# Kernel tuning notes

Measured on AMD Instinct MI355X. Metric: run time of the kernel, lower is better.

Reference implementation:

```python
import jax, jax.numpy as jnp
import numpy as np

EPS = 1e-5
DN = ('NCHW', 'OIHW', 'NCHW')

def _conv(x, w):
    return jax.lax.conv_general_dilated(x, w, (1, 1), 'VALID', dimension_numbers=DN)

def _bn4(x, g, b, m, v):
    # BatchNorm2d in eval mode, per-channel over NCHW
    inv = g / jnp.sqrt(v + EPS)
    return x * inv[None, :, None, None] + (b - m * inv)[None, :, None, None]

def _bn1(x, g, b, m, v):
    inv = g / jnp.sqrt(v + EPS)
    return x * inv[None, :] + (b - m * inv)[None, :]

def _hardtanh(x):
    return jnp.clip(x, -1.0, 1.0)

def _sign(x):
    return jnp.sign(x)

def _maxpool2(x):
    return jax.lax.reduce_window(x, -jnp.inf, jax.lax.max,
                                 (1, 1, 2, 2), (1, 1, 2, 2), 'VALID')

def setup_inputs() -> dict:
    key = jax.random.key(0)
    ks = jax.random.split(key, 20)
    B = 8192
    d = {
        'x': jax.random.normal(ks[0], (B, 8, 16, 16), jnp.float32),
        'w0': jax.random.normal(ks[1], (32, 8, 3, 3), jnp.float32) * 0.1,
        'b0': jax.random.normal(ks[2], (32,), jnp.float32) * 0.1,
        'g1': jax.random.uniform(ks[3], (32,), jnp.float32, 0.5, 1.5),
        'be1': jax.random.normal(ks[4], (32,), jnp.float32) * 0.1,
        'm1': jax.random.normal(ks[5], (32,), jnp.float32) * 0.1,
        'v1': jax.random.uniform(ks[6], (32,), jnp.float32, 0.5, 1.5),
        'w2': jax.random.normal(ks[7], (32, 32, 3, 3), jnp.float32) * 0.1,
        'g2': jax.random.uniform(ks[8], (32,), jnp.float32, 0.5, 1.5),
        'be2': jax.random.normal(ks[9], (32,), jnp.float32) * 0.1,
        'm2': jax.random.normal(ks[10], (32,), jnp.float32) * 0.1,
        'v2': jax.random.uniform(ks[11], (32,), jnp.float32, 0.5, 1.5),
        'w_fc': jax.random.normal(ks[12], (516, 1152), jnp.float32) * 0.03,
        'g3': jax.random.uniform(ks[13], (516,), jnp.float32, 0.5, 1.5),
        'be3': jax.random.normal(ks[14], (516,), jnp.float32) * 0.1,
        'm3': jax.random.normal(ks[15], (516,), jnp.float32) * 0.1,
        'v3': jax.random.uniform(ks[16], (516,), jnp.float32, 0.5, 1.5),
        'w_last': jax.random.normal(ks[17], (10, 516), jnp.float32) * 0.05,
        'b_last': jax.random.normal(ks[18], (10,), jnp.float32) * 0.05,
    }
    return d

def reference(x, w0, b0, g1, be1, m1, v1, w2, g2, be2, m2, v2,
              w_fc, g3, be3, m3, v3, w_last, b_last):
    # initial float conv + BN + Hardtanh
    h = _conv(x, w0) + b0[None, :, None, None]          # [B,32,14,14]
    h = _hardtanh(_bn4(h, g1, be1, m1, v1))
    # binarized conv (sign(input), sign(weight), no bias)
    h = _conv(_sign(h), _sign(w2))                      # [B,32,12,12]
    h = _hardtanh(_bn4(h, g2, be2, m2, v2))
    h = _maxpool2(h)                                    # [B,32,6,6]
    # dropout is identity in eval mode
    h = h.reshape(h.shape[0], -1)                       # [B,1152]
    # binarized linear (no bias)
    h = _sign(h) @ _sign(w_fc).T                        # [B,516]
    h = _hardtanh(_bn1(h, g3, be3, m3, v3))
    return h @ w_last.T + b_last[None, :]               # [B,10]
```

## Files before the change

kernel.cpp:

```cpp
#include <hip/hip_runtime.h>
#include <cstdint>

#define EPSF 1e-5f

typedef __attribute__((ext_vector_type(8))) short short8;
typedef __attribute__((ext_vector_type(4))) float f32x4;
typedef __attribute__((ext_vector_type(4))) unsigned int u32x4;

__device__ inline uint32_t bf16rne(float x) {
    uint32_t u = __builtin_bit_cast(uint32_t, x);
    return (u + 0x7fffu + ((u >> 16) & 1u)) >> 16;
}
__device__ inline float bf16f(uint32_t b) {
    return __builtin_bit_cast(float, b << 16);
}

__global__ __launch_bounds__(256) void prep_kernel(
    const float* __restrict__ w2, const float* __restrict__ wfc,
    const float* __restrict__ g3, const float* __restrict__ be3,
    const float* __restrict__ m3, const float* __restrict__ v3,
    const float* __restrict__ wlast,
    const float* __restrict__ w0, const float* __restrict__ b0,
    const float* __restrict__ g1, const float* __restrict__ be1,
    const float* __restrict__ m1, const float* __restrict__ v1,
    uint32_t* __restrict__ w2bits, uint32_t* __restrict__ wfcb,
    float* __restrict__ inv3p, float* __restrict__ sh3p, float* __restrict__ wlt,
    uint32_t* __restrict__ bfrag, float2* __restrict__ bn1c)
{
    int id = blockIdx.x * 256 + threadIdx.x;
    if (id < 288) {
        int co = id / 9, r = id % 9;
        uint32_t b = 0;
        for (int ci = 0; ci < 32; ci++)
            b |= (uint32_t)(w2[(co * 32 + ci) * 9 + r] < 0.f) << ci;
        w2bits[id] = b;
        return;
    }
    id -= 288;
    if (id < 36 * 576) {
        int j = id / 36, pos = id % 36;
        uint32_t b = 0;
        if (j < 516) {
            const float* row = wfc + j * 1152 + pos;
            for (int c = 0; c < 32; c++)
                b |= (uint32_t)(row[c * 36] < 0.f) << c;
        }
        wfcb[pos * 576 + j] = b;
        return;
    }
    id -= 36 * 576;
    if (id < 576) {
        float iv = 0.f, sh = 0.f;
        if (id < 516) {
            iv = g3[id] / sqrtf(__fadd_rn(v3[id], EPSF));
            sh = __fsub_rn(be3[id], __fmul_rn(m3[id], iv));
        }
        inv3p[id] = iv; sh3p[id] = sh;
        return;
    }
    id -= 576;
    if (id < 5760) {
        int k = id / 576, j = id % 576;
        wlt[id] = (j < 516) ? wlast[k * 516 + j] : 0.f;
        return;
    }
    id -= 5760;
    if (id < 768) {
        int L = id / 12, r = id % 12;
        int nt = r / 6, s = (r % 6) / 2, h = r & 1;
        int g = L >> 4, n = L & 15;
        int tap = 4 * s + g;
        uint32_t d[4] = {0, 0, 0, 0};
        if (tap < 9) {
            int co = nt * 16 + n;
            for (int j2 = 0; j2 < 4; j2++) {
                float wa = w0[co * 72 + (2 * j2) * 9 + tap];
                float wb = w0[co * 72 + (2 * j2 + 1) * 9 + tap];
                uint32_t ha = bf16rne(wa), hb = bf16rne(wb);
                uint32_t va, vb;
                if (h == 0) { va = ha; vb = hb; }
                else { va = bf16rne(wa - bf16f(ha)); vb = bf16rne(wb - bf16f(hb)); }
                d[j2] = va | (vb << 16);
            }
        }
        *(u32x4*)(bfrag + id * 4) = (u32x4){d[0], d[1], d[2], d[3]};
        return;
    }
    id -= 768;
    if (id < 32) {
        float iv = g1[id] / sqrtf(__fadd_rn(v1[id], EPSF));
        float sh = __fsub_rn(be1[id], __fmul_rn(m1[id], iv));
        float off = __fadd_rn(__fmul_rn(b0[id], iv), sh);
        bn1c[id] = make_float2(iv, off);
    }
}

__device__ __noinline__ bool recheck_sign(const float* __restrict__ xim,
                                          const float* __restrict__ w0,
                                          int py, int px, int co,
                                          float ivc, float offc)
{
    double ad = 0.0;
    for (int ci = 0; ci < 8; ci++)
        for (int ky = 0; ky < 3; ky++)
            for (int kx = 0; kx < 3; kx++)
                ad = fma((double)xim[ci * 256 + (py + ky) * 16 + px + kx],
                         (double)w0[co * 72 + ci * 9 + ky * 3 + kx], ad);
    return (ad * (double)ivc + (double)offc) < 0.0;
}

__global__ __launch_bounds__(128, 4) void convAB(
    const float* __restrict__ x, const float* __restrict__ w0,
    const uint32_t* __restrict__ bfrag, const float2* __restrict__ bn1c,
    const uint32_t* __restrict__ w2bits,
    const float* __restrict__ g2, const float* __restrict__ be2,
    const float* __restrict__ m2, const float* __restrict__ v2,
    uint32_t* __restrict__ fcin)
{
    __shared__ __align__(16) char simg[9216];
    __shared__ __align__(8) uint32_t s1l[196];

    const int t = threadIdx.x;
    const int wv = t >> 6, lane = t & 63;
    const int img = blockIdx.x;
    const float* xim = x + img * 2048;
    char* hib = simg;
    char* lob = simg + 4608;

    const int g = lane >> 4;
    const int n = lane & 15;

    short8 Bh[2][3], Bl[2][3];
    {
        const uint32_t* bb = bfrag + lane * 48;
        #pragma unroll
        for (int nt = 0; nt < 2; nt++)
            #pragma unroll
            for (int s = 0; s < 3; s++) {
                Bh[nt][s] = *(const short8*)(bb + (nt * 6 + s * 2) * 4);
                Bl[nt][s] = *(const short8*)(bb + (nt * 6 + s * 2 + 1) * 4);
            }
    }
    const float2 bnA = bn1c[n], bnB = bn1c[16 + n];

    #pragma unroll
    for (int qq = 0; qq < 2; qq++) {
        int pos = lane + 64 * (2 * wv + qq);
        uint32_t hw[4], lw[4];
        #pragma unroll
        for (int j2 = 0; j2 < 4; j2++) {
            float a = xim[(2 * j2) * 256 + pos];
            float b = xim[(2 * j2 + 1) * 256 + pos];
            uint32_t ha = bf16rne(a), hb = bf16rne(b);
            uint32_t la = bf16rne(a - bf16f(ha)), lb = bf16rne(b - bf16f(hb));
            hw[j2] = ha | (hb << 16);
            lw[j2] = la | (lb << 16);
        }
        *(u32x4*)(hib + pos * 16) = (u32x4){hw[0], hw[1], hw[2], hw[3]};
        *(u32x4*)(lob + pos * 16) = (u32x4){lw[0], lw[1], lw[2], lw[3]};
    }
    if (lane < 32) {
        char* gp = (wv == 0) ? hib : lob;
        *(u32x4*)(gp + (256 + lane) * 16) = (u32x4){0, 0, 0, 0};
    }

    int koff[3];
    #pragma unroll
    for (int s = 0; s < 3; s++) {
        int tap = 4 * s + g;
        koff[s] = (tap < 9) ? ((tap / 3) * 16 + (tap % 3)) * 16 : 0;
    }

    __syncthreads();

    for (int tile = wv; tile < 13; tile += 2) {
        int posA = tile * 16 + n;
        int pyA = posA / 14, pxA = posA - pyA * 14;
        int sl = (pyA * 16 + pxA) * 16;

        f32x4 acc0 = {0.f, 0.f, 0.f, 0.f}, acc1 = {0.f, 0.f, 0.f, 0.f};
        #pragma unroll
        for (int s = 0; s < 3; s++) {
            short8 Ah = *(const short8*)(hib + sl + koff[s]);
            short8 Al = *(const short8*)(lob + sl + koff[s]);
            acc0 = __builtin_amdgcn_mfma_f32_16x16x32_bf16(Al, Bh[0][s], acc0, 0, 0, 0);
            acc0 = __builtin_amdgcn_mfma_f32_16x16x32_bf16(Ah, Bl[0][s], acc0, 0, 0, 0);
            acc0 = __builtin_amdgcn_mfma_f32_16x16x32_bf16(Ah, Bh[0][s], acc0, 0, 0, 0);
            acc1 = __builtin_amdgcn_mfma_f32_16x16x32_bf16(Al, Bh[1][s], acc1, 0, 0, 0);
            acc1 = __builtin_amdgcn_mfma_f32_16x16x32_bf16(Ah, Bl[1][s], acc1, 0, 0, 0);
            acc1 = __builtin_amdgcn_mfma_f32_16x16x32_bf16(Ah, Bh[1][s], acc1, 0, 0, 0);
        }

        #pragma unroll
        for (int r = 0; r < 4; r++) {
            int pos = tile * 16 + 4 * g + r;
            float yv0 = fmaf(acc0[r], bnA.x, bnA.y);
            float yv1 = fmaf(acc1[r], bnB.x, bnB.y);
            bool bit0, bit1;
            if (__builtin_expect(pos < 196 && fabsf(yv0) < 3e-4f, 0)) {
                int py = pos / 14, px = pos - py * 14;
                bit0 = recheck_sign(xim, w0, py, px, n, bnA.x, bnA.y);
            } else bit0 = (yv0 < 0.f);
            if (__builtin_expect(pos < 196 && fabsf(yv1) < 3e-4f, 0)) {
                int py = pos / 14, px = pos - py * 14;
                bit1 = recheck_sign(xim, w0, py, px, 16 + n, bnB.x, bnB.y);
            } else bit1 = (yv1 < 0.f);
            unsigned long long m0 = __ballot(bit0);
            unsigned long long m1 = __ballot(bit1);
            uint32_t word = (uint32_t)((m0 >> (16 * g)) & 0xffffull)
                          | ((uint32_t)((m1 >> (16 * g)) & 0xffffull) << 16);
            if (n == 0 && pos < 196) s1l[pos] = word;
        }
    }

    __syncthreads();

    {
        const int c = lane & 31, h = lane >> 5;
        uint32_t wr[9];
        #pragma unroll
        for (int k = 0; k < 9; k++) wr[k] = w2bits[c * 9 + k];
        float ivv = g2[c] / sqrtf(__fadd_rn(v2[c], EPSF));
        float shv = __fsub_rn(be2[c], __fmul_rn(m2[c], ivv));
        uint32_t* outp = fcin + img * 36;
        const int cb0 = 6 * h;

        for (int yy = 0; yy < 3; yy++) {
            const int y2 = 3 * wv + yy;
            const int rbase = 2 * y2 * 14;
            uint32_t win[4][4];
            #pragma unroll
            for (int rr = 0; rr < 4; rr++) {
                uint2 a = *(const uint2*)&s1l[rbase + rr * 14 + cb0];
                uint2 b = *(const uint2*)&s1l[rbase + rr * 14 + cb0 + 2];
                win[rr][0] = a.x; win[rr][1] = a.y; win[rr][2] = b.x; win[rr][3] = b.y;
            }
            for (int step = 0; step < 3; step++) {
                if (step > 0) {
                    #pragma unroll
                    for (int rr = 0; rr < 4; rr++) {
                        win[rr][0] = win[rr][2]; win[rr][1] = win[rr][3];
                        uint2 b = *(const uint2*)&s1l[rbase + rr * 14 + cb0 + 2 * step + 2];
                        win[rr][2] = b.x; win[rr][3] = b.y;
                    }
                }
                int mx = -10000;
                #pragma unroll
                for (int dy = 0; dy < 2; dy++)
                    #pragma unroll
                    for (int dx = 0; dx < 2; dx++) {
                        int p = 0;
                        #pragma unroll
                        for (int ky = 0; ky < 3; ky++)
                            #pragma unroll
                            for (int kx = 0; kx < 3; kx++)
                                p += __popc(win[dy + ky][dx + kx] ^ wr[ky * 3 + kx]);
                        mx = max(mx, 288 - 2 * p);
                    }
                float yv = __fadd_rn(__fmul_rn((float)mx, ivv), shv);
                unsigned long long mb = __ballot(yv < 0.f);
                if (lane == 0)  outp[y2 * 6 + step]     = (uint32_t)mb;
                if (lane == 32) outp[y2 * 6 + step + 3] = (uint32_t)(mb >> 32);
            }
        }
    }
}

__global__ __launch_bounds__(256) void fcC(
    const uint32_t* __restrict__ fcin, const uint32_t* __restrict__ wfcb,
    const float* __restrict__ inv3p, const float* __restrict__ sh3p,
    const float* __restrict__ wlt, const float* __restrict__ blast,
    float* __restrict__ out)
{
    __shared__ uint32_t l_in[288];
    const int t = threadIdx.x, wid = t >> 6, lane = t & 63;

    for (int i = t; i < 288; i += 256) l_in[i] = fcin[blockIdx.x * 288 + i];
    __syncthreads();

    const int b0i = blockIdx.x * 8 + wid * 2;
    const uint32_t* in0 = &l_in[wid * 72];

    int pc0[9], pc1[9];
    #pragma unroll
    for (int q = 0; q < 9; q++) { pc0[q] = 0; pc1[q] = 0; }

    for (int w = 0; w < 36; w++) {
        uint32_t i0 = in0[w], i1 = in0[36 + w];
        const uint32_t* wf = wfcb + w * 576 + lane;
        #pragma unroll
        for (int q = 0; q < 9; q++) {
            uint32_t f = wf[q * 64];
            pc0[q] += __popc(i0 ^ f);
            pc1[q] += __popc(i1 ^ f);
        }
    }

    float oa[2][10];
    #pragma unroll
    for (int b = 0; b < 2; b++)
        #pragma unroll
        for (int k = 0; k < 10; k++) oa[b][k] = 0.f;

    #pragma unroll
    for (int q = 0; q < 9; q++) {
        int j = lane + 64 * q;
        float ivv = inv3p[j], shv = sh3p[j];
        float t0 = fminf(1.f, fmaxf(-1.f, __fadd_rn(__fmul_rn((float)(1152 - 2 * pc0[q]), ivv), shv)));
        float t1 = fminf(1.f, fmaxf(-1.f, __fadd_rn(__fmul_rn((float)(1152 - 2 * pc1[q]), ivv), shv)));
        #pragma unroll
        for (int k = 0; k < 10; k++) {
            float wv = wlt[k * 576 + j];
            oa[0][k] = fmaf(t0, wv, oa[0][k]);
            oa[1][k] = fmaf(t1, wv, oa[1][k]);
        }
    }

    #pragma unroll
    for (int m = 1; m < 64; m <<= 1)
        #pragma unroll
        for (int b = 0; b < 2; b++)
            #pragma unroll
            for (int k = 0; k < 10; k++)
                oa[b][k] += __shfl_xor(oa[b][k], m, 64);

    if (lane == 0) {
        for (int b = 0; b < 2; b++)
            for (int k = 0; k < 10; k++)
                out[(b0i + b) * 10 + k] = oa[b][k] + blast[k];
    }
}

extern "C" void kernel_launch(void* const* d_in, const int* in_sizes, int n_in,
                              void* d_out, int out_size, void* d_ws, size_t ws_size,
                              hipStream_t stream)
{
    (void)in_sizes; (void)n_in; (void)out_size; (void)ws_size;
    const float* x     = (const float*)d_in[0];
    const float* w0    = (const float*)d_in[1];
    const float* b0    = (const float*)d_in[2];
    const float* g1    = (const float*)d_in[3];
    const float* be1   = (const float*)d_in[4];
    const float* m1    = (const float*)d_in[5];
    const float* v1    = (const float*)d_in[6];
    const float* w2    = (const float*)d_in[7];
    const float* g2    = (const float*)d_in[8];
    const float* be2   = (const float*)d_in[9];
    const float* m2    = (const float*)d_in[10];
    const float* v2    = (const float*)d_in[11];
    const float* wfc   = (const float*)d_in[12];
    const float* g3    = (const float*)d_in[13];
    const float* be3   = (const float*)d_in[14];
    const float* m3    = (const float*)d_in[15];
    const float* v3    = (const float*)d_in[16];
    const float* wlast = (const float*)d_in[17];
    const float* blast = (const float*)d_in[18];

    char* ws = (char*)d_ws;
    uint32_t* fcin   = (uint32_t*)(ws + 6422528);
    uint32_t* w2bits = (uint32_t*)(ws + 7602176);
    uint32_t* wfcb   = (uint32_t*)(ws + 7603328);
    float*    inv3p  = (float*)(ws + 7686272);
    float*    sh3p   = (float*)(ws + 7688576);
    float*    wlt    = (float*)(ws + 7690880);
    uint32_t* bfrag  = (uint32_t*)(ws + 7713920);
    float2*   bn1c   = (float2*)(ws + 7726208);

    prep_kernel<<<110, 256, 0, stream>>>(w2, wfc, g3, be3, m3, v3, wlast,
                                         w0, b0, g1, be1, m1, v1,
                                         w2bits, wfcb, inv3p, sh3p, wlt,
                                         bfrag, bn1c);
    convAB<<<8192, 128, 0, stream>>>(x, w0, bfrag, bn1c,
                                     w2bits, g2, be2, m2, v2, fcin);
    fcC<<<1024, 256, 0, stream>>>(fcin, wfcb, inv3p, sh3p, wlt, blast, (float*)d_out);
}
```

Measured before the change: 215.0 us.

## Process four images per block with double-buffered async global-to-LDS prefetch

The conv kernel now loops over four images per block instead of one. It prefetches the next image's raw input into a second LDS buffer with global_load_lds while the current image runs through the MFMA and popcount stages. This is meant to hide global load latency and spread the per-block B-fragment and BN setup over more work. In exchange it adds LDS use, launches fewer blocks, and relies on correct wait semantics for the asynchronous LDS loads.

```diff
diff --git a/kernel.cpp b/kernel.cpp
--- a/kernel.cpp
+++ b/kernel.cpp
@@ -13,6 +13,13 @@
 }
 __device__ inline float bf16f(uint32_t b) {
     return __builtin_bit_cast(float, b << 16);
+}
+
+__device__ inline void gl_lds16(const void* g, void* l) {
+    __builtin_amdgcn_global_load_lds(
+        (__attribute__((address_space(1))) void*)(uintptr_t)(g),
+        (__attribute__((address_space(3))) void*)(l),
+        16, 0, 0);
 }
 
 __global__ __launch_bounds__(256) void prep_kernel(
@@ -118,12 +125,11 @@
     uint32_t* __restrict__ fcin)
 {
     __shared__ __align__(16) char simg[9216];
+    __shared__ __align__(16) uint32_t rawb[2][2048];
     __shared__ __align__(8) uint32_t s1l[196];
 
     const int t = threadIdx.x;
     const int wv = t >> 6, lane = t & 63;
-    const int img = blockIdx.x;
-    const float* xim = x + img * 2048;
     char* hib = simg;
     char* lob = simg + 4608;
 
@@ -143,22 +149,6 @@
     }
     const float2 bnA = bn1c[n], bnB = bn1c[16 + n];
 
-    #pragma unroll
-    for (int qq = 0; qq < 2; qq++) {
-        int pos = lane + 64 * (2 * wv + qq);
-        uint32_t hw[4], lw[4];
-        #pragma unroll
-        for (int j2 = 0; j2 < 4; j2++) {
-            float a = xim[(2 * j2) * 256 + pos];
-            float b = xim[(2 * j2 + 1) * 256 + pos];
-            uint32_t ha = bf16rne(a), hb = bf16rne(b);
-            uint32_t la = bf16rne(a - bf16f(ha)), lb = bf16rne(b - bf16f(hb));
-            hw[j2] = ha | (hb << 16);
-            lw[j2] = la | (lb << 16);
-        }
-        *(u32x4*)(hib + pos * 16) = (u32x4){hw[0], hw[1], hw[2], hw[3]};
-        *(u32x4*)(lob + pos * 16) = (u32x4){lw[0], lw[1], lw[2], lw[3]};
-    }
     if (lane < 32) {
         char* gp = (wv == 0) ? hib : lob;
         *(u32x4*)(gp + (256 + lane) * 16) = (u32x4){0, 0, 0, 0};
@@ -171,98 +161,144 @@
         koff[s] = (tap < 9) ? ((tap / 3) * 16 + (tap % 3)) * 16 : 0;
     }
 
-    __syncthreads();
-
-    for (int tile = wv; tile < 13; tile += 2) {
-        int posA = tile * 16 + n;
-        int pyA = posA / 14, pxA = posA - pyA * 14;
-        int sl = (pyA * 16 + pxA) * 16;
-
-        f32x4 acc0 = {0.f, 0.f, 0.f, 0.f}, acc1 = {0.f, 0.f, 0.f, 0.f};
-        #pragma unroll
-        for (int s = 0; s < 3; s++) {
-            short8 Ah = *(const short8*)(hib + sl + koff[s]);
-            short8 Al = *(const short8*)(lob + sl + koff[s]);
-            acc0 = __builtin_amdgcn_mfma_f32_16x16x32_bf16(Al, Bh[0][s], acc0, 0, 0, 0);
-            acc0 = __builtin_amdgcn_mfma_f32_16x16x32_bf16(Ah, Bl[0][s], acc0, 0, 0, 0);
-            acc0 = __builtin_amdgcn_mfma_f32_16x16x32_bf16(Ah, Bh[0][s], acc0, 0, 0, 0);
-            acc1 = __builtin_amdgcn_mfma_f32_16x16x32_bf16(Al, Bh[1][s], acc1, 0, 0, 0);
-            acc1 = __builtin_amdgcn_mfma_f32_16x16x32_bf16(Ah, Bl[1][s], acc1, 0, 0, 0);
-            acc1 = __builtin_amdgcn_mfma_f32_16x16x32_bf16(Ah, Bh[1][s], acc1, 0, 0, 0);
-        }
-
-        #pragma unroll
-        for (int r = 0; r < 4; r++) {
-            int pos = tile * 16 + 4 * g + r;
-            float yv0 = fmaf(acc0[r], bnA.x, bnA.y);
-            float yv1 = fmaf(acc1[r], bnB.x, bnB.y);
-            bool bit0, bit1;
-            if (__builtin_expect(pos < 196 && fabsf(yv0) < 3e-4f, 0)) {
-                int py = pos / 14, px = pos - py * 14;
-                bit0 = recheck_sign(xim, w0, py, px, n, bnA.x, bnA.y);
-            } else bit0 = (yv0 < 0.f);
-            if (__builtin_expect(pos < 196 && fabsf(yv1) < 3e-4f, 0)) {
-                int py = pos / 14, px = pos - py * 14;
-                bit1 = recheck_sign(xim, w0, py, px, 16 + n, bnB.x, bnB.y);
-            } else bit1 = (yv1 < 0.f);
-            unsigned long long m0 = __ballot(bit0);
-            unsigned long long m1 = __ballot(bit1);
-            uint32_t word = (uint32_t)((m0 >> (16 * g)) & 0xffffull)
-                          | ((uint32_t)((m1 >> (16 * g)) & 0xffffull) << 16);
-            if (n == 0 && pos < 196) s1l[pos] = word;
-        }
-    }
-
-    __syncthreads();
-
     {
-        const int c = lane & 31, h = lane >> 5;
-        uint32_t wr[9];
-        #pragma unroll
-        for (int k = 0; k < 9; k++) wr[k] = w2bits[c * 9 + k];
-        float ivv = g2[c] / sqrtf(__fadd_rn(v2[c], EPSF));
-        float shv = __fsub_rn(be2[c], __fmul_rn(m2[c], ivv));
-        uint32_t* outp = fcin + img * 36;
-        const int cb0 = 6 * h;
-
-        for (int yy = 0; yy < 3; yy++) {
-            const int y2 = 3 * wv + yy;
-            const int rbase = 2 * y2 * 14;
-            uint32_t win[4][4];
-            #pragma unroll
-            for (int rr = 0; rr < 4; rr++) {
-                uint2 a = *(const uint2*)&s1l[rbase + rr * 14 + cb0];
-                uint2 b = *(const uint2*)&s1l[rbase + rr * 14 + cb0 + 2];
-                win[rr][0] = a.x; win[rr][1] = a.y; win[rr][2] = b.x; win[rr][3] = b.y;
-            }
-            for (int step = 0; step < 3; step++) {
-                if (step > 0) {
+        const float* xg = x + (size_t)(blockIdx.x * 4) * 2048;
+        #pragma unroll
+        for (int j = 0; j < 4; j++)
+            gl_lds16(xg + (wv * 4 + j) * 256 + lane * 4,
+                     (char*)&rawb[0][(wv * 4 + j) * 256]);
+    }
+
+    int cur = 0;
+    for (int i = 0; i < 4; ++i) {
+        const int img = blockIdx.x * 4 + i;
+        const float* xim = x + (size_t)img * 2048;
+
+        __syncthreads();
+
+        {
+            const uint32_t* rp = rawb[cur];
+            #pragma unroll
+            for (int qq = 0; qq < 2; qq++) {
+                int pos = lane + 64 * (2 * wv + qq);
+                uint32_t hw[4], lw[4];
+                #pragma unroll
+                for (int j2 = 0; j2 < 4; j2++) {
+                    float a = __builtin_bit_cast(float, rp[(2 * j2) * 256 + pos]);
+                    float b = __builtin_bit_cast(float, rp[(2 * j2 + 1) * 256 + pos]);
+                    uint32_t ha = bf16rne(a), hb = bf16rne(b);
+                    uint32_t la = bf16rne(a - bf16f(ha)), lb = bf16rne(b - bf16f(hb));
+                    hw[j2] = ha | (hb << 16);
+                    lw[j2] = la | (lb << 16);
+                }
+                *(u32x4*)(hib + pos * 16) = (u32x4){hw[0], hw[1], hw[2], hw[3]};
+                *(u32x4*)(lob + pos * 16) = (u32x4){lw[0], lw[1], lw[2], lw[3]};
+            }
+        }
+
+        __syncthreads();
+
+        if (i < 3) {
+            const float* xg = x + (size_t)(img + 1) * 2048;
+            #pragma unroll
+            for (int j = 0; j < 4; j++)
+                gl_lds16(xg + (wv * 4 + j) * 256 + lane * 4,
+                         (char*)&rawb[cur ^ 1][(wv * 4 + j) * 256]);
+        }
+
+        for (int tile = wv; tile < 13; tile += 2) {
+            int posA = tile * 16 + n;
+            int pyA = posA / 14, pxA = posA - pyA * 14;
+            int sl = (pyA * 16 + pxA) * 16;
+
+            f32x4 acc0 = {0.f, 0.f, 0.f, 0.f}, acc1 = {0.f, 0.f, 0.f, 0.f};
+            #pragma unroll
+            for (int s = 0; s < 3; s++) {
+                short8 Ah = *(const short8*)(hib + sl + koff[s]);
+                short8 Al = *(const short8*)(lob + sl + koff[s]);
+                acc0 = __builtin_amdgcn_mfma_f32_16x16x32_bf16(Al, Bh[0][s], acc0, 0, 0, 0);
+                acc0 = __builtin_amdgcn_mfma_f32_16x16x32_bf16(Ah, Bl[0][s], acc0, 0, 0, 0);
+                acc0 = __builtin_amdgcn_mfma_f32_16x16x32_bf16(Ah, Bh[0][s], acc0, 0, 0, 0);
+                acc1 = __builtin_amdgcn_mfma_f32_16x16x32_bf16(Al, Bh[1][s], acc1, 0, 0, 0);
+                acc1 = __builtin_amdgcn_mfma_f32_16x16x32_bf16(Ah, Bl[1][s], acc1, 0, 0, 0);
+                acc1 = __builtin_amdgcn_mfma_f32_16x16x32_bf16(Ah, Bh[1][s], acc1, 0, 0, 0);
+            }
+
+            #pragma unroll
+            for (int r = 0; r < 4; r++) {
+                int pos = tile * 16 + 4 * g + r;
+                float yv0 = fmaf(acc0[r], bnA.x, bnA.y);
+                float yv1 = fmaf(acc1[r], bnB.x, bnB.y);
+                bool bit0, bit1;
+                if (__builtin_expect(pos < 196 && fabsf(yv0) < 3e-4f, 0)) {
+                    int py = pos / 14, px = pos - py * 14;
+                    bit0 = recheck_sign(xim, w0, py, px, n, bnA.x, bnA.y);
+                } else bit0 = (yv0 < 0.f);
+                if (__builtin_expect(pos < 196 && fabsf(yv1) < 3e-4f, 0)) {
+                    int py = pos / 14, px = pos - py * 14;
+                    bit1 = recheck_sign(xim, w0, py, px, 16 + n, bnB.x, bnB.y);
+                } else bit1 = (yv1 < 0.f);
+                unsigned long long m0 = __ballot(bit0);
+                unsigned long long m1 = __ballot(bit1);
+                uint32_t word = (uint32_t)((m0 >> (16 * g)) & 0xffffull)
+                              | ((uint32_t)((m1 >> (16 * g)) & 0xffffull) << 16);
+                if (n == 0 && pos < 196) s1l[pos] = word;
+            }
+        }
+
+        __syncthreads();
+
+        {
+            const int c = lane & 31, h = lane >> 5;
+            uint32_t wr[9];
+            #pragma unroll
+            for (int k = 0; k < 9; k++) wr[k] = w2bits[c * 9 + k];
+            float ivv = g2[c] / sqrtf(__fadd_rn(v2[c], EPSF));
+            float shv = __fsub_rn(be2[c], __fmul_rn(m2[c], ivv));
+            uint32_t* outp = fcin + img * 36;
+            const int cb0 = 6 * h;
+
+            for (int yy = 0; yy < 3; yy++) {
+                const int y2 = 3 * wv + yy;
+                const int rbase = 2 * y2 * 14;
+                uint32_t win[4][4];
+                #pragma unroll
+                for (int rr = 0; rr < 4; rr++) {
+                    uint2 a = *(const uint2*)&s1l[rbase + rr * 14 + cb0];
+                    uint2 b = *(const uint2*)&s1l[rbase + rr * 14 + cb0 + 2];
+                    win[rr][0] = a.x; win[rr][1] = a.y; win[rr][2] = b.x; win[rr][3] = b.y;
+                }
+                for (int step = 0; step < 3; step++) {
+                    if (step > 0) {
+                        #pragma unroll
+                        for (int rr = 0; rr < 4; rr++) {
+                            win[rr][0] = win[rr][2]; win[rr][1] = win[rr][3];
+                            uint2 b = *(const uint2*)&s1l[rbase + rr * 14 + cb0 + 2 * step + 2];
+                            win[rr][2] = b.x; win[rr][3] = b.y;
+                        }
+                    }
+                    int mx = -10000;
                     #pragma unroll
-                    for (int rr = 0; rr < 4; rr++) {
-                        win[rr][0] = win[rr][2]; win[rr][1] = win[rr][3];
-                        uint2 b = *(const uint2*)&s1l[rbase + rr * 14 + cb0 + 2 * step + 2];
-                        win[rr][2] = b.x; win[rr][3] = b.y;
-                    }
+                    for (int dy = 0; dy < 2; dy++)
+                        #pragma unroll
+                        for (int dx = 0; dx < 2; dx++) {
+                            int p = 0;
+                            #pragma unroll
+                            for (int ky = 0; ky < 3; ky++)
+                                #pragma unroll
+                                for (int kx = 0; kx < 3; kx++)
+                                    p += __popc(win[dy + ky][dx + kx] ^ wr[ky * 3 + kx]);
+                            mx = max(mx, 288 - 2 * p);
+                        }
+                    float yv = __fadd_rn(__fmul_rn((float)mx, ivv), shv);
+                    unsigned long long mb = __ballot(yv < 0.f);
+                    if (lane == 0)  outp[y2 * 6 + step]     = (uint32_t)mb;
+                    if (lane == 32) outp[y2 * 6 + step + 3] = (uint32_t)(mb >> 32);
                 }
-                int mx = -10000;
-                #pragma unroll
-                for (int dy = 0; dy < 2; dy++)
-                    #pragma unroll
-                    for (int dx = 0; dx < 2; dx++) {
-                        int p = 0;
-                        #pragma unroll
-                        for (int ky = 0; ky < 3; ky++)
-                            #pragma unroll
-                            for (int kx = 0; kx < 3; kx++)
-                                p += __popc(win[dy + ky][dx + kx] ^ wr[ky * 3 + kx]);
-                        mx = max(mx, 288 - 2 * p);
-                    }
-                float yv = __fadd_rn(__fmul_rn((float)mx, ivv), shv);
-                unsigned long long mb = __ballot(yv < 0.f);
-                if (lane == 0)  outp[y2 * 6 + step]     = (uint32_t)mb;
-                if (lane == 32) outp[y2 * 6 + step + 3] = (uint32_t)(mb >> 32);
-            }
-        }
+            }
+        }
+
+        cur ^= 1;
     }
 }
 
@@ -370,7 +406,7 @@
                                          w0, b0, g1, be1, m1, v1,
                                          w2bits, wfcb, inv3p, sh3p, wlt,
                                          bfrag, bn1c);
-    convAB<<<8192, 128, 0, stream>>>(x, w0, bfrag, bn1c,
+    convAB<<<2048, 128, 0, stream>>>(x, w0, bfrag, bn1c,
                                      w2bits, g2, be2, m2, v2, fcin);
     fcC<<<1024, 256, 0, stream>>>(fcin, wfcb, inv3p, sh3p, wlt, blast, (float*)d_out);
 }
```

Result: slower. 245.8 us (+14.3%).
